# Optimization experiments

Measured on AMD Instinct MI355X. Metric: run time of the kernel, lower is better.

The kernel has to match this reference:

```python
import jax, jax.numpy as jnp
import numpy as np

B, C, H, W = 8, 256, 48, 48
RED = 1  # reduction
CR = C // RED
CG = C // 4  # fuse gate hidden channels


def conv1x1(x, w):
    # x: [B,C,H,W], w: [O,C] -> [B,O,H,W]
    return jnp.einsum('oc,bchw->bohw', w, x)


def conv3x3(x, w, b):
    # x: [B,Ci,H,W], w: [O,Ci,3,3], b: [O]
    y = jax.lax.conv_general_dilated(
        x, w, window_strides=(1, 1), padding='SAME',
        dimension_numbers=('NCHW', 'OIHW', 'NCHW'))
    return y + b[None, :, None, None]


def cross_attention(source, guidance, wq, wk, wv, bv, gamma):
    b, c, h, w = source.shape
    hw = h * w
    Q = conv1x1(source, wq).reshape(b, -1, hw)      # [B,CR,HW]
    K = conv1x1(guidance, wk).reshape(b, -1, hw)    # [B,CR,HW]
    V = (conv1x1(guidance, wv) + bv[None, :, None, None]).reshape(b, c, hw)
    energy = jnp.einsum('bqn,bqm->bnm', Q, K)       # [B,HW,HW]
    attn = jax.nn.softmax(energy, axis=-1)
    out = jnp.einsum('bcm,bnm->bcn', V, attn)       # [B,C,HW]
    return gamma * out.reshape(b, c, h, w) + source


def setup_inputs() -> dict:
    key = jax.random.key(0)
    ks = jax.random.split(key, 16)
    s = lambda fan_in: 1.0 / np.sqrt(fan_in)
    d = {
        'x1': jax.random.normal(ks[0], (B, C, H, W), jnp.float32),
        'x2': jax.random.normal(ks[1], (B, C, H, W), jnp.float32),
        'wq1': jax.random.normal(ks[2], (CR, C), jnp.float32) * s(C),
        'wk1': jax.random.normal(ks[3], (CR, C), jnp.float32) * s(C),
        'wv1': jax.random.normal(ks[4], (C, C), jnp.float32) * s(C),
        'bv1': jax.random.normal(ks[5], (C,), jnp.float32) * s(C),
        'gamma1': jax.random.normal(ks[6], (1,), jnp.float32) * 0.1,
        'wq2': jax.random.normal(ks[7], (CR, C), jnp.float32) * s(C),
        'wk2': jax.random.normal(ks[8], (CR, C), jnp.float32) * s(C),
        'wv2': jax.random.normal(ks[9], (C, C), jnp.float32) * s(C),
        'bv2': jax.random.normal(ks[10], (C,), jnp.float32) * s(C),
        'gamma2': jax.random.normal(ks[11], (1,), jnp.float32) * 0.1,
        'fw1': jax.random.normal(ks[12], (CG, 2 * C, 3, 3), jnp.float32) * s(2 * C * 9),
        'fb1': jnp.zeros((CG,), jnp.float32),
        'fw2': jax.random.normal(ks[13], (2, CG, 3, 3), jnp.float32) * s(CG * 9),
        'fb2': jnp.zeros((2,), jnp.float32),
    }
    return d


def reference(x1, x2, wq1, wk1, wv1, bv1, gamma1, wq2, wk2, wv2, bv2, gamma2,
              fw1, fb1, fw2, fb2):
    att_x1 = cross_attention(x1, x2, wq1, wk1, wv1, bv1, gamma1)
    att_x2 = cross_attention(x2, x1, wq2, wk2, wv2, bv2, gamma2)
    cat = jnp.concatenate([att_x1, att_x2], axis=1)  # [B,2C,H,W]
    h = jax.nn.relu(conv3x3(cat, fw1, fb1))
    gates = jax.nn.softmax(conv3x3(h, fw2, fb2), axis=1)  # [B,2,H,W]
    return gates[:, 0:1] * att_x1 + gates[:, 1:2] * att_x2
```

## Files before the change

kernel.cpp:

```cpp
#include <hip/hip_runtime.h>

namespace {

constexpr int BATCH = 8;
constexpr int CH    = 256;
constexpr int HW    = 2304;
constexpr int IMG   = 48;
constexpr int CG    = 64;

typedef __bf16 bf16x8 __attribute__((ext_vector_type(8)));
typedef __bf16 bf16x4 __attribute__((ext_vector_type(4)));
typedef float  f32x4  __attribute__((ext_vector_type(4)));

constexpr int ROWB = 40;
constexpr int PSTRD = 136;
constexpr int CSTR = 40;
constexpr int KQ_ELE = 8192;

constexpr size_t BF_SLAB = (size_t)BATCH * HW * CH * 2;
constexpr size_t QT1_OFF = 0;
constexpr size_t KT1_OFF = 1 * BF_SLAB;
constexpr size_t VB1_OFF = 2 * BF_SLAB;
constexpr size_t QT2_OFF = 3 * BF_SLAB;
constexpr size_t KT2_OFF = 4 * BF_SLAB;
constexpr size_t VB2_OFF = 5 * BF_SLAB;
constexpr size_t AT_OFF  = 6 * BF_SLAB;
constexpr size_t A1_OFF  = AT_OFF + (size_t)BATCH * HW * 512 * 2;
constexpr size_t A2_OFF  = A1_OFF + (size_t)BATCH * CH * HW * 4;
constexpr size_t HB_OFF  = A2_OFF + (size_t)BATCH * CH * HW * 4;
constexpr size_t G0_OFF  = HB_OFF + (size_t)BATCH * CG * HW * 4;
constexpr size_t WT_OFF  = G0_OFF + (size_t)BATCH * HW * 4;

__device__ __forceinline__ void dma16(const __bf16* g, __bf16* l) {
    __builtin_amdgcn_global_load_lds(
        (const __attribute__((address_space(1))) void*)g,
        (__attribute__((address_space(3))) void*)l,
        16, 0, 0);
}

__device__ __forceinline__ void issue_k_dma(const __bf16* __restrict__ KTb,
                                            __bf16* Kslot, int m0_i, int qq,
                                            int w, int lane) {
    const int lrow = lane >> 3;
    const int lg   = (lane & 7) ^ lrow;
    const int colb = qq * 64 + lg * 8;
#pragma unroll
    for (int qi = 0; qi < 4; ++qi) {
        const int row = (w * 4 + qi) * 8 + lrow;
        dma16(KTb + (size_t)(m0_i + row) * CH + colb,
              Kslot + (w * 4 + qi) * 512);
    }
}

__device__ __forceinline__ void stage_f32(const float* __restrict__ src, size_t srcStride,
                                          __bf16* dst, int t) {
    const int r = t & 127, s = t >> 7;
    const float4* sp = reinterpret_cast<const float4*>(src + (size_t)r * srcStride + s * 16);
    float4 f0 = sp[0], f1 = sp[1], f2 = sp[2], f3 = sp[3];
    bf16x8 v0, v1;
    v0[0]=(__bf16)f0.x; v0[1]=(__bf16)f0.y; v0[2]=(__bf16)f0.z; v0[3]=(__bf16)f0.w;
    v0[4]=(__bf16)f1.x; v0[5]=(__bf16)f1.y; v0[6]=(__bf16)f1.z; v0[7]=(__bf16)f1.w;
    v1[0]=(__bf16)f2.x; v1[1]=(__bf16)f2.y; v1[2]=(__bf16)f2.z; v1[3]=(__bf16)f2.w;
    v1[4]=(__bf16)f3.x; v1[5]=(__bf16)f3.y; v1[6]=(__bf16)f3.z; v1[7]=(__bf16)f3.w;
    bf16x8* dp = reinterpret_cast<bf16x8*>(dst + r * ROWB + s * 16);
    dp[0] = v0;
    dp[1] = v1;
}

__device__ __forceinline__ void frag_step(const __bf16* As, const __bf16* Bs,
                                          f32x4 (&acc)[4][4], int lane, int wm, int wn) {
    const int r = lane & 15, g = lane >> 4;
    bf16x8 a[4], b[4];
#pragma unroll
    for (int i = 0; i < 4; ++i) {
        a[i] = *reinterpret_cast<const bf16x8*>(As + (wm * 64 + i * 16 + r) * ROWB + g * 8);
        b[i] = *reinterpret_cast<const bf16x8*>(Bs + (wn * 64 + i * 16 + r) * ROWB + g * 8);
    }
#pragma unroll
    for (int i = 0; i < 4; ++i)
#pragma unroll
        for (int j = 0; j < 4; ++j)
            acc[i][j] = __builtin_amdgcn_mfma_f32_16x16x32_bf16(a[i], b[j], acc[i][j], 0, 0, 0);
}

__global__ __launch_bounds__(256) void proj3_mfma(
    const float* __restrict__ Xsrc, const float* __restrict__ Xg,
    const float* __restrict__ wq, const float* __restrict__ wk,
    const float* __restrict__ wv, const float* __restrict__ bv,
    __bf16* __restrict__ QT, __bf16* __restrict__ KT, __bf16* __restrict__ VB)
{
    __shared__ __bf16 As[128 * ROWB];
    __shared__ __bf16 Bs[128 * ROWB];
    const int p = blockIdx.z >> 3;
    const int b = blockIdx.z & 7;
    const float* W = (p == 0) ? wq : (p == 1) ? wk : wv;
    const float* X = (p == 0) ? Xsrc : Xg;
    const float* Xb = X + (size_t)b * CH * HW;

    const int t = threadIdx.x;
    const int lane = t & 63, wid = t >> 6;
    const int wm = wid >> 1, wn = wid & 1;
    const int m0 = blockIdx.y * 128, n0 = blockIdx.x * 128;

    f32x4 acc[4][4] = {};
    const int nB = t & 127, halfB = t >> 7;

    for (int k0 = 0; k0 < CH; k0 += 32) {
        stage_f32(W + (size_t)m0 * CH + k0, CH, As, t);
        float v[16];
#pragma unroll
        for (int kk = 0; kk < 16; ++kk)
            v[kk] = Xb[(size_t)(k0 + halfB * 16 + kk) * HW + n0 + nB];
        bf16x8 p0, p1;
#pragma unroll
        for (int kk = 0; kk < 8; ++kk) { p0[kk] = (__bf16)v[kk]; p1[kk] = (__bf16)v[kk + 8]; }
        bf16x8* dp = reinterpret_cast<bf16x8*>(Bs + nB * ROWB + halfB * 16);
        dp[0] = p0; dp[1] = p1;
        __syncthreads();
        frag_step(As, Bs, acc, lane, wm, wn);
        __syncthreads();
    }

    const int g = lane >> 4, r = lane & 15;
    if (p < 2) {
        __bf16* T = (p == 0) ? QT : KT;
#pragma unroll
        for (int mi = 0; mi < 4; ++mi)
#pragma unroll
            for (int nj = 0; nj < 4; ++nj) {
                const int mb = m0 + wm * 64 + mi * 16 + g * 4;
                const int n  = n0 + wn * 64 + nj * 16 + r;
                bf16x4 pk;
#pragma unroll
                for (int q = 0; q < 4; ++q) pk[q] = (__bf16)acc[mi][nj][q];
                *reinterpret_cast<bf16x4*>(T + ((size_t)b * HW + n) * CH + mb) = pk;
            }
    } else {
#pragma unroll
        for (int mi = 0; mi < 4; ++mi)
#pragma unroll
            for (int nj = 0; nj < 4; ++nj) {
                const int mb = m0 + wm * 64 + mi * 16 + g * 4;
                const int n  = n0 + wn * 64 + nj * 16 + r;
#pragma unroll
                for (int q = 0; q < 4; ++q)
                    VB[((size_t)b * CH + mb + q) * HW + n] = (__bf16)(acc[mi][nj][q] + bv[mb + q]);
            }
    }
}

__global__ __launch_bounds__(256, 2) void fused_flash(
    const __bf16* __restrict__ QT1, const __bf16* __restrict__ KT1, const __bf16* __restrict__ VB1,
    const __bf16* __restrict__ QT2, const __bf16* __restrict__ KT2, const __bf16* __restrict__ VB2,
    const float* __restrict__ x1, const float* __restrict__ x2,
    const float* __restrict__ g1, const float* __restrict__ g2,
    float* __restrict__ A1, float* __restrict__ A2, __bf16* __restrict__ AT)
{
    __shared__ __bf16 Ks[3 * KQ_ELE];
    __shared__ __bf16 P_lds[64 * PSTRD];
    __shared__ float  sc_lds[64];

    const int bid  = blockIdx.x;
    const int work = (bid & 7) * 72 + (bid >> 3);
    const int z = work / 36, ntile = work - z * 36;

    const int att = z >> 3, b = z & 7;
    const __bf16* QT = att ? QT2 : QT1;
    const __bf16* KT = att ? KT2 : KT1;
    const __bf16* VB = att ? VB2 : VB1;
    const float* src = att ? x2 : x1;
    const float* gmp = att ? g2 : g1;
    float* A         = att ? A2 : A1;
    const int aoff   = att ? CH : 0;

    const int t = threadIdx.x, lane = t & 63, w = t >> 6;
    const int r = lane & 15, g = lane >> 4;
    const int rs7 = r & 7;
    const int n0 = ntile * 64;
    const __bf16* KTb = KT + (size_t)b * HW * CH;
    const __bf16* VBb = VB + (size_t)b * CH * HW;

    bf16x8 qf[8];
    {
        const __bf16* qrow = QT + ((size_t)b * HW + n0 + w * 16 + r) * CH;
#pragma unroll
        for (int kc = 0; kc < 8; ++kc)
            qf[kc] = *reinterpret_cast<const bf16x8*>(qrow + kc * 32 + g * 8);
    }

    issue_k_dma(KTb, Ks, 0, 0, w, lane);
    issue_k_dma(KTb, Ks + KQ_ELE, 0, 1, w, lane);

    float m_run = -3.0e38f;
    float s_run = 0.f;
    f32x4 accO[4][4] = {};
    int base_t = 0;

    for (int tile = 0; tile < 18; ++tile) {
        const int m0 = tile * 128;
        f32x4 accS[8] = {};
#pragma unroll
        for (int q = 0; q < 4; ++q) {
            asm volatile("s_waitcnt vmcnt(4)\n\ts_barrier" ::: "memory");
            {
                int qq_i = q + 2;
                int m0_i = m0;
                if (qq_i >= 4) { qq_i -= 4; m0_i = (tile == 17) ? 0 : m0 + 128; }
                int slot_i = base_t + q + 2;
                if (slot_i >= 3) slot_i -= 3;
                if (slot_i >= 3) slot_i -= 3;
                issue_k_dma(KTb, Ks + slot_i * KQ_ELE, m0_i, qq_i, w, lane);
            }
            int slot = base_t + q;
            if (slot >= 3) slot -= 3;
            const __bf16* Kq = Ks + slot * KQ_ELE;
            __builtin_amdgcn_s_setprio(1);
#pragma unroll
            for (int kk = 0; kk < 2; ++kk) {
                const bf16x8 qv = qf[q * 2 + kk];
                const int swz = ((kk * 4 + g) ^ rs7) * 8;
#pragma unroll
                for (int j = 0; j < 8; ++j) {
                    const bf16x8 kf = *reinterpret_cast<const bf16x8*>(
                        Kq + (j * 16 + r) * 64 + swz);
                    accS[j] = __builtin_amdgcn_mfma_f32_16x16x32_bf16(kf, qv, accS[j], 0, 0, 0);
                }
            }
            __builtin_amdgcn_s_setprio(0);
        }
        {
            float mj[8];
#pragma unroll
            for (int j = 0; j < 8; ++j)
                mj[j] = fmaxf(fmaxf(accS[j][0], accS[j][1]), fmaxf(accS[j][2], accS[j][3]));
            float m03 = fmaxf(fmaxf(mj[0], mj[1]), fmaxf(mj[2], mj[3]));
            float m47 = fmaxf(fmaxf(mj[4], mj[5]), fmaxf(mj[6], mj[7]));
            float tmax = fmaxf(m03, m47);
            tmax = fmaxf(tmax, __shfl_xor(tmax, 16));
            tmax = fmaxf(tmax, __shfl_xor(tmax, 32));
            const float nm = fmaxf(m_run, tmax);
            float tsj[8];
#pragma unroll
            for (int j = 0; j < 8; ++j) {
                const float pe0 = __expf(accS[j][0] - nm);
                const float pe1 = __expf(accS[j][1] - nm);
                const float pe2 = __expf(accS[j][2] - nm);
                const float pe3 = __expf(accS[j][3] - nm);
                tsj[j] = (pe0 + pe1) + (pe2 + pe3);
                bf16x4 pk;
                pk[0] = (__bf16)pe0; pk[1] = (__bf16)pe1;
                pk[2] = (__bf16)pe2; pk[3] = (__bf16)pe3;
                *reinterpret_cast<bf16x4*>(
                    P_lds + (w * 16 + r) * PSTRD + j * 16 + g * 4) = pk;
            }
            float ts = ((tsj[0] + tsj[1]) + (tsj[2] + tsj[3])) +
                       ((tsj[4] + tsj[5]) + (tsj[6] + tsj[7]));
            ts += __shfl_xor(ts, 16);
            ts += __shfl_xor(ts, 32);
            const float scale = __expf(m_run - nm);
            s_run = s_run * scale + ts;
            m_run = nm;
            if (lane < 16) sc_lds[w * 16 + r] = scale;
        }
        asm volatile("s_waitcnt lgkmcnt(0)\n\ts_barrier" ::: "memory");
        {
            float scj[4];
#pragma unroll
            for (int j = 0; j < 4; ++j) scj[j] = sc_lds[j * 16 + r];
#pragma unroll
            for (int i = 0; i < 4; ++i)
#pragma unroll
                for (int j = 0; j < 4; ++j)
#pragma unroll
                    for (int q = 0; q < 4; ++q) accO[i][j][q] *= scj[j];
        }
        __builtin_amdgcn_s_setprio(1);
#pragma unroll
        for (int half = 0; half < 2; ++half) {
#pragma unroll
            for (int kk = 0; kk < 2; ++kk) {
                bf16x8 av[4], bp[4];
#pragma unroll
                for (int i = 0; i < 4; ++i)
                    av[i] = *reinterpret_cast<const bf16x8*>(
                        VBb + (size_t)(w * 64 + i * 16 + r) * HW + m0 + half * 64 + kk * 32 + g * 8);
#pragma unroll
                for (int j = 0; j < 4; ++j)
                    bp[j] = *reinterpret_cast<const bf16x8*>(
                        P_lds + (j * 16 + r) * PSTRD + half * 64 + kk * 32 + g * 8);
#pragma unroll
                for (int i = 0; i < 4; ++i)
#pragma unroll
                    for (int j = 0; j < 4; ++j)
                        accO[i][j] = __builtin_amdgcn_mfma_f32_16x16x32_bf16(
                            av[i], bp[j], accO[i][j], 0, 0, 0);
            }
        }
        __builtin_amdgcn_s_setprio(0);
        base_t += 1;
        if (base_t == 3) base_t = 0;
    }

    if (lane < 16) sc_lds[w * 16 + r] = 1.f / s_run;
    __syncthreads();
    float IS_l[4];
#pragma unroll
    for (int j = 0; j < 4; ++j) IS_l[j] = sc_lds[j * 16 + r];
    const float gm = gmp[0];
#pragma unroll
    for (int i = 0; i < 4; ++i)
#pragma unroll
        for (int j = 0; j < 4; ++j) {
            const int cb = w * 64 + i * 16 + g * 4;
            const int n  = n0 + j * 16 + r;
            const float sc = gm * IS_l[j];
            float vals[4];
#pragma unroll
            for (int q = 0; q < 4; ++q) {
                const size_t idx = ((size_t)b * CH + cb + q) * HW + n;
                vals[q] = sc * accO[i][j][q] + src[idx];
                A[idx] = vals[q];
            }
            bf16x4 pk;
#pragma unroll
            for (int q = 0; q < 4; ++q) pk[q] = (__bf16)vals[q];
            *reinterpret_cast<bf16x4*>(AT + ((size_t)b * HW + n) * 512 + aoff + cb) = pk;
        }
}

__global__ __launch_bounds__(256) void wprep(const float* __restrict__ fw1,
                                             __bf16* __restrict__ WT)
{
    const int i = blockIdx.x * 256 + threadIdx.x;
    const int tap = i >> 15;
    const int rem = i & 32767;
    const int m = rem >> 9, c = rem & 511;
    WT[i] = (__bf16)fw1[(size_t)m * 4608 + c * 9 + tap];
}

__global__ __launch_bounds__(256) void conv1_v2(
    const __bf16* __restrict__ AT, const __bf16* __restrict__ WT,
    float* __restrict__ P4)
{
    __shared__ __bf16 A9[9 * 64 * CSTR];
    __shared__ __bf16 HALO[240 * CSTR];
    const int kc = blockIdx.y, b = blockIdx.z, n0 = blockIdx.x * 128;
    const int t = threadIdx.x, lane = t & 63, wid = t >> 6;
    const int r = lane & 15, g = lane >> 4;

    int yj[2], xj[2];
#pragma unroll
    for (int j = 0; j < 2; ++j) {
        const int p = n0 + wid * 32 + j * 16 + r;
        yj[j] = p / IMG; xj[j] = p - yj[j] * IMG;
    }

    f32x4 acc[4][2] = {};

#pragma unroll 1
    for (int st = 0; st < 4; ++st) {
        const int cbase = kc * 128 + st * 32;
        if (t < 240) {
            const int nn = n0 - 56 + t;
            bf16x8 h0 = {}, h1 = {}, h2 = {}, h3 = {};
            if (nn >= 0 && nn < HW) {
                const bf16x8* sp = reinterpret_cast<const bf16x8*>(
                    AT + ((size_t)b * HW + nn) * 512 + cbase);
                h0 = sp[0]; h1 = sp[1]; h2 = sp[2]; h3 = sp[3];
            }
            bf16x8* dp = reinterpret_cast<bf16x8*>(HALO + t * CSTR);
            dp[0] = h0; dp[1] = h1; dp[2] = h2; dp[3] = h3;
        }
        {
            const int m = t >> 2, seg = t & 3;
#pragma unroll
            for (int tap = 0; tap < 9; ++tap)
                *reinterpret_cast<bf16x8*>(A9 + (tap * 64 + m) * CSTR + seg * 8) =
                    *reinterpret_cast<const bf16x8*>(WT + ((size_t)tap * 64 + m) * 512 + cbase + seg * 8);
        }
        __syncthreads();
#pragma unroll 1
        for (int tap = 0; tap < 9; ++tap) {
            const int dy = tap / 3 - 1;
            const int dx = tap - (tap / 3) * 3 - 1;
            bf16x8 bb[2];
#pragma unroll
            for (int j = 0; j < 2; ++j) {
                const bool valid = ((unsigned)(yj[j] + dy) < (unsigned)IMG) &&
                                   ((unsigned)(xj[j] + dx) < (unsigned)IMG);
                const int row = wid * 32 + j * 16 + r + 56 + dy * IMG + dx;
                bf16x8 v = {};
                if (valid) v = *reinterpret_cast<const bf16x8*>(HALO + row * CSTR + g * 8);
                bb[j] = v;
            }
            bf16x8 a[4];
#pragma unroll
            for (int i = 0; i < 4; ++i)
                a[i] = *reinterpret_cast<const bf16x8*>(A9 + (tap * 64 + i * 16 + r) * CSTR + g * 8);
#pragma unroll
            for (int i = 0; i < 4; ++i)
#pragma unroll
                for (int j = 0; j < 2; ++j)
                    acc[i][j] = __builtin_amdgcn_mfma_f32_16x16x32_bf16(a[i], bb[j], acc[i][j], 0, 0, 0);
        }
        __syncthreads();
    }
#pragma unroll
    for (int mi = 0; mi < 4; ++mi)
#pragma unroll
        for (int nj = 0; nj < 2; ++nj) {
            const int m = mi * 16 + g * 4;
            const int n = n0 + wid * 32 + nj * 16 + r;
#pragma unroll
            for (int q = 0; q < 4; ++q)
                P4[(((size_t)kc * BATCH + b) * CG + m + q) * HW + n] = acc[mi][nj][q];
        }
}

__global__ __launch_bounds__(256) void reduce_hb(
    const float* __restrict__ P4, const float* __restrict__ fb1,
    float* __restrict__ HB)
{
    const int idx = blockIdx.x * 256 + threadIdx.x;
    constexpr size_t STRIDE = (size_t)BATCH * CG * HW;
    const int m = (idx / HW) & 63;
    float s = P4[idx] + P4[idx + STRIDE] + P4[idx + 2 * STRIDE] + P4[idx + 3 * STRIDE];
    HB[idx] = fmaxf(s + fb1[m], 0.f);
}

__global__ __launch_bounds__(256) void gates_v2(
    const float* __restrict__ hbuf, const float* __restrict__ fw2,
    const float* __restrict__ fb2, float* __restrict__ g0buf)
{
    __shared__ float w2s[1152];
    __shared__ float par[2][4][64];
    const int t = threadIdx.x;
    for (int i = t; i < 1152; i += 256) w2s[i] = fw2[i];
    __syncthreads();
    const int px = t & 63, grp = t >> 6;
    const int idx = blockIdx.x * 64 + px;
    const int b = idx / HW;
    const int n = idx - b * HW;
    const int y = n / IMG, x = n - (n / IMG) * IMG;
    float c0 = 0.f, c1 = 0.f;
    const float* hb = hbuf + ((size_t)b * CG + grp * 16) * HW;
    for (int ci = 0; ci < 16; ++ci) {
        const float* hp = hb + (size_t)ci * HW;
        const float* w0 = &w2s[(grp * 16 + ci) * 9];
        const float* w1 = &w2s[576 + (grp * 16 + ci) * 9];
#pragma unroll
        for (int tap = 0; tap < 9; ++tap) {
            const int dy = tap / 3 - 1, dx = tap % 3 - 1;
            const int yy = y + dy, xx = x + dx;
            if (yy >= 0 && yy < IMG && xx >= 0 && xx < IMG) {
                const float hv = hp[yy * IMG + xx];
                c0 = fmaf(hv, w0[tap], c0);
                c1 = fmaf(hv, w1[tap], c1);
            }
        }
    }
    par[0][grp][px] = c0;
    par[1][grp][px] = c1;
    __syncthreads();
    if (t < 64) {
        const float s0 = par[0][0][t] + par[0][1][t] + par[0][2][t] + par[0][3][t] + fb2[0];
        const float s1 = par[1][0][t] + par[1][1][t] + par[1][2][t] + par[1][3][t] + fb2[1];
        g0buf[blockIdx.x * 64 + t] = 1.f / (1.f + __expf(s1 - s0));
    }
}

__global__ __launch_bounds__(256) void blend_kernel(
    const float* __restrict__ att1, const float* __restrict__ att2,
    const float* __restrict__ g0buf, float* __restrict__ out)
{
    const int i = blockIdx.x * 256 + threadIdx.x;
    const int r = i / 576;
    const int q = i - r * 576;
    const int b = r >> 8;
    const float4 a1 = reinterpret_cast<const float4*>(att1)[i];
    const float4 a2 = reinterpret_cast<const float4*>(att2)[i];
    const float4 g  = *reinterpret_cast<const float4*>(&g0buf[(size_t)b * HW + q * 4]);
    float4 o;
    o.x = g.x * a1.x + (1.f - g.x) * a2.x;
    o.y = g.y * a1.y + (1.f - g.y) * a2.y;
    o.z = g.z * a1.z + (1.f - g.z) * a2.z;
    o.w = g.w * a1.w + (1.f - g.w) * a2.w;
    reinterpret_cast<float4*>(out)[i] = o;
}

}

extern "C" void kernel_launch(void* const* d_in, const int* in_sizes, int n_in,
                              void* d_out, int out_size, void* d_ws, size_t ws_size,
                              hipStream_t stream)
{
    const float* x1  = (const float*)d_in[0];
    const float* x2  = (const float*)d_in[1];
    const float* wq1 = (const float*)d_in[2];
    const float* wk1 = (const float*)d_in[3];
    const float* wv1 = (const float*)d_in[4];
    const float* bv1 = (const float*)d_in[5];
    const float* g1  = (const float*)d_in[6];
    const float* wq2 = (const float*)d_in[7];
    const float* wk2 = (const float*)d_in[8];
    const float* wv2 = (const float*)d_in[9];
    const float* bv2 = (const float*)d_in[10];
    const float* g2  = (const float*)d_in[11];
    const float* fw1 = (const float*)d_in[12];
    const float* fb1 = (const float*)d_in[13];
    const float* fw2 = (const float*)d_in[14];
    const float* fb2 = (const float*)d_in[15];
    float* out = (float*)d_out;
    char*  wsb = (char*)d_ws;

    __bf16* QT1 = (__bf16*)(wsb + QT1_OFF);
    __bf16* KT1 = (__bf16*)(wsb + KT1_OFF);
    __bf16* VB1 = (__bf16*)(wsb + VB1_OFF);
    __bf16* QT2 = (__bf16*)(wsb + QT2_OFF);
    __bf16* KT2 = (__bf16*)(wsb + KT2_OFF);
    __bf16* VB2 = (__bf16*)(wsb + VB2_OFF);
    __bf16* AT  = (__bf16*)(wsb + AT_OFF);
    float*  A1  = (float*)(wsb + A1_OFF);
    float*  A2  = (float*)(wsb + A2_OFF);
    float*  HB  = (float*)(wsb + HB_OFF);
    float*  G0  = (float*)(wsb + G0_OFF);
    __bf16* WT  = (__bf16*)(wsb + WT_OFF);
    float*  P4  = (float*)(wsb + QT1_OFF);

    (void)in_sizes; (void)n_in; (void)out_size; (void)ws_size;

    proj3_mfma<<<dim3(18, 2, 24), 256, 0, stream>>>(x1, x2, wq1, wk1, wv1, bv1, QT1, KT1, VB1);
    proj3_mfma<<<dim3(18, 2, 24), 256, 0, stream>>>(x2, x1, wq2, wk2, wv2, bv2, QT2, KT2, VB2);
    wprep<<<dim3(1152), 256, 0, stream>>>(fw1, WT);

    fused_flash<<<dim3(576), 256, 0, stream>>>(
        QT1, KT1, VB1, QT2, KT2, VB2, x1, x2, g1, g2, A1, A2, AT);

    conv1_v2<<<dim3(18, 4, 8), 256, 0, stream>>>(AT, WT, P4);
    reduce_hb<<<dim3(4608), 256, 0, stream>>>(P4, fb1, HB);
    gates_v2<<<dim3(288), 256, 0, stream>>>(HB, fw2, fb2, G0);
    blend_kernel<<<dim3(4608), 256, 0, stream>>>(A1, A2, G0, out);
}
```

Before: 404.1 us.

## Keep attention probabilities in registers and read K directly from global memory

Removes all shared memory from the fused flash-attention kernel. K tiles are now loaded straight from global memory instead of through a triple-buffered DMA ring, and the probability tile is permuted between lanes with shuffles instead of being staged in LDS. Each wave now owns its 16 queries across all 256 channels, which removes the block barriers. The cost is that every wave reloads the full K and V tiles from global memory (four times the traffic), and the epilogue writes are scalar and less coalesced.

```diff
diff --git a/kernel.cpp b/kernel.cpp
--- a/kernel.cpp
+++ b/kernel.cpp
@@ -11,11 +11,10 @@
 typedef __bf16 bf16x8 __attribute__((ext_vector_type(8)));
 typedef __bf16 bf16x4 __attribute__((ext_vector_type(4)));
 typedef float  f32x4  __attribute__((ext_vector_type(4)));
+typedef unsigned u32x4 __attribute__((ext_vector_type(4)));
 
 constexpr int ROWB = 40;
-constexpr int PSTRD = 136;
 constexpr int CSTR = 40;
-constexpr int KQ_ELE = 8192;
 
 constexpr size_t BF_SLAB = (size_t)BATCH * HW * CH * 2;
 constexpr size_t QT1_OFF = 0;
@@ -31,25 +30,10 @@
 constexpr size_t G0_OFF  = HB_OFF + (size_t)BATCH * CG * HW * 4;
 constexpr size_t WT_OFF  = G0_OFF + (size_t)BATCH * HW * 4;
 
-__device__ __forceinline__ void dma16(const __bf16* g, __bf16* l) {
-    __builtin_amdgcn_global_load_lds(
-        (const __attribute__((address_space(1))) void*)g,
-        (__attribute__((address_space(3))) void*)l,
-        16, 0, 0);
-}
-
-__device__ __forceinline__ void issue_k_dma(const __bf16* __restrict__ KTb,
-                                            __bf16* Kslot, int m0_i, int qq,
-                                            int w, int lane) {
-    const int lrow = lane >> 3;
-    const int lg   = (lane & 7) ^ lrow;
-    const int colb = qq * 64 + lg * 8;
-#pragma unroll
-    for (int qi = 0; qi < 4; ++qi) {
-        const int row = (w * 4 + qi) * 8 + lrow;
-        dma16(KTb + (size_t)(m0_i + row) * CH + colb,
-              Kslot + (w * 4 + qi) * 512);
-    }
+__device__ __forceinline__ unsigned pk2(float lo, float hi) {
+    unsigned short a = __builtin_bit_cast(unsigned short, (__bf16)lo);
+    unsigned short b = __builtin_bit_cast(unsigned short, (__bf16)hi);
+    return (unsigned)a | ((unsigned)b << 16);
 }
 
 __device__ __forceinline__ void stage_f32(const float* __restrict__ src, size_t srcStride,
@@ -156,10 +140,6 @@
     const float* __restrict__ g1, const float* __restrict__ g2,
     float* __restrict__ A1, float* __restrict__ A2, __bf16* __restrict__ AT)
 {
-    __shared__ __bf16 Ks[3 * KQ_ELE];
-    __shared__ __bf16 P_lds[64 * PSTRD];
-    __shared__ float  sc_lds[64];
-
     const int bid  = blockIdx.x;
     const int work = (bid & 7) * 72 + (bid >> 3);
     const int z = work / 36, ntile = work - z * 36;
@@ -175,11 +155,13 @@
 
     const int t = threadIdx.x, lane = t & 63, w = t >> 6;
     const int r = lane & 15, g = lane >> 4;
-    const int rs7 = r & 7;
     const int n0 = ntile * 64;
     const __bf16* KTb = KT + (size_t)b * HW * CH;
     const __bf16* VBb = VB + (size_t)b * CH * HW;
 
+    const int sb  = r + (((lane >> 4) & 1) << 5);
+    const bool ghi = ((lane >> 5) & 1);
+
     bf16x8 qf[8];
     {
         const __bf16* qrow = QT + ((size_t)b * HW + n0 + w * 16 + r) * CH;
@@ -188,46 +170,25 @@
             qf[kc] = *reinterpret_cast<const bf16x8*>(qrow + kc * 32 + g * 8);
     }
 
-    issue_k_dma(KTb, Ks, 0, 0, w, lane);
-    issue_k_dma(KTb, Ks + KQ_ELE, 0, 1, w, lane);
-
     float m_run = -3.0e38f;
     float s_run = 0.f;
-    f32x4 accO[4][4] = {};
-    int base_t = 0;
+    f32x4 accO2[16] = {};
 
     for (int tile = 0; tile < 18; ++tile) {
         const int m0 = tile * 128;
         f32x4 accS[8] = {};
 #pragma unroll
-        for (int q = 0; q < 4; ++q) {
-            asm volatile("s_waitcnt vmcnt(4)\n\ts_barrier" ::: "memory");
-            {
-                int qq_i = q + 2;
-                int m0_i = m0;
-                if (qq_i >= 4) { qq_i -= 4; m0_i = (tile == 17) ? 0 : m0 + 128; }
-                int slot_i = base_t + q + 2;
-                if (slot_i >= 3) slot_i -= 3;
-                if (slot_i >= 3) slot_i -= 3;
-                issue_k_dma(KTb, Ks + slot_i * KQ_ELE, m0_i, qq_i, w, lane);
-            }
-            int slot = base_t + q;
-            if (slot >= 3) slot -= 3;
-            const __bf16* Kq = Ks + slot * KQ_ELE;
-            __builtin_amdgcn_s_setprio(1);
-#pragma unroll
-            for (int kk = 0; kk < 2; ++kk) {
-                const bf16x8 qv = qf[q * 2 + kk];
-                const int swz = ((kk * 4 + g) ^ rs7) * 8;
-#pragma unroll
-                for (int j = 0; j < 8; ++j) {
-                    const bf16x8 kf = *reinterpret_cast<const bf16x8*>(
-                        Kq + (j * 16 + r) * 64 + swz);
-                    accS[j] = __builtin_amdgcn_mfma_f32_16x16x32_bf16(kf, qv, accS[j], 0, 0, 0);
-                }
-            }
-            __builtin_amdgcn_s_setprio(0);
-        }
+        for (int kk = 0; kk < 8; ++kk) {
+            const bf16x8 qv = qf[kk];
+#pragma unroll
+            for (int j = 0; j < 8; ++j) {
+                const bf16x8 kf = *reinterpret_cast<const bf16x8*>(
+                    KTb + (size_t)(m0 + j * 16 + r) * CH + kk * 32 + g * 8);
+                accS[j] = __builtin_amdgcn_mfma_f32_16x16x32_bf16(kf, qv, accS[j], 0, 0, 0);
+            }
+        }
+        unsigned dwj[8][2];
+        float scale;
         {
             float mj[8];
 #pragma unroll
@@ -247,85 +208,74 @@
                 const float pe2 = __expf(accS[j][2] - nm);
                 const float pe3 = __expf(accS[j][3] - nm);
                 tsj[j] = (pe0 + pe1) + (pe2 + pe3);
-                bf16x4 pk;
-                pk[0] = (__bf16)pe0; pk[1] = (__bf16)pe1;
-                pk[2] = (__bf16)pe2; pk[3] = (__bf16)pe3;
-                *reinterpret_cast<bf16x4*>(
-                    P_lds + (w * 16 + r) * PSTRD + j * 16 + g * 4) = pk;
+                dwj[j][0] = pk2(pe0, pe1);
+                dwj[j][1] = pk2(pe2, pe3);
             }
             float ts = ((tsj[0] + tsj[1]) + (tsj[2] + tsj[3])) +
                        ((tsj[4] + tsj[5]) + (tsj[6] + tsj[7]));
             ts += __shfl_xor(ts, 16);
             ts += __shfl_xor(ts, 32);
-            const float scale = __expf(m_run - nm);
+            scale = __expf(m_run - nm);
             s_run = s_run * scale + ts;
             m_run = nm;
-            if (lane < 16) sc_lds[w * 16 + r] = scale;
-        }
-        asm volatile("s_waitcnt lgkmcnt(0)\n\ts_barrier" ::: "memory");
+        }
         {
-            float scj[4];
-#pragma unroll
-            for (int j = 0; j < 4; ++j) scj[j] = sc_lds[j * 16 + r];
-#pragma unroll
-            for (int i = 0; i < 4; ++i)
-#pragma unroll
-                for (int j = 0; j < 4; ++j)
-#pragma unroll
-                    for (int q = 0; q < 4; ++q) accO[i][j][q] *= scj[j];
+            float sc4[4];
+#pragma unroll
+            for (int q = 0; q < 4; ++q) sc4[q] = __shfl(scale, g * 4 + q);
+#pragma unroll
+            for (int cb = 0; cb < 16; ++cb)
+#pragma unroll
+                for (int q = 0; q < 4; ++q) accO2[cb][q] *= sc4[q];
+        }
+        bf16x8 pa[4];
+#pragma unroll
+        for (int ks = 0; ks < 4; ++ks) {
+            const unsigned a0 = (unsigned)__shfl((int)dwj[2 * ks][0], sb);
+            const unsigned b0 = (unsigned)__shfl((int)dwj[2 * ks + 1][0], sb);
+            const unsigned a1 = (unsigned)__shfl((int)dwj[2 * ks][1], sb);
+            const unsigned b1 = (unsigned)__shfl((int)dwj[2 * ks + 1][1], sb);
+            const unsigned a2 = (unsigned)__shfl((int)dwj[2 * ks][0], sb + 16);
+            const unsigned b2 = (unsigned)__shfl((int)dwj[2 * ks + 1][0], sb + 16);
+            const unsigned a3 = (unsigned)__shfl((int)dwj[2 * ks][1], sb + 16);
+            const unsigned b3 = (unsigned)__shfl((int)dwj[2 * ks + 1][1], sb + 16);
+            u32x4 dd;
+            dd.x = ghi ? b0 : a0;
+            dd.y = ghi ? b1 : a1;
+            dd.z = ghi ? b2 : a2;
+            dd.w = ghi ? b3 : a3;
+            pa[ks] = __builtin_bit_cast(bf16x8, dd);
         }
         __builtin_amdgcn_s_setprio(1);
 #pragma unroll
-        for (int half = 0; half < 2; ++half) {
-#pragma unroll
-            for (int kk = 0; kk < 2; ++kk) {
-                bf16x8 av[4], bp[4];
-#pragma unroll
-                for (int i = 0; i < 4; ++i)
-                    av[i] = *reinterpret_cast<const bf16x8*>(
-                        VBb + (size_t)(w * 64 + i * 16 + r) * HW + m0 + half * 64 + kk * 32 + g * 8);
-#pragma unroll
-                for (int j = 0; j < 4; ++j)
-                    bp[j] = *reinterpret_cast<const bf16x8*>(
-                        P_lds + (j * 16 + r) * PSTRD + half * 64 + kk * 32 + g * 8);
-#pragma unroll
-                for (int i = 0; i < 4; ++i)
-#pragma unroll
-                    for (int j = 0; j < 4; ++j)
-                        accO[i][j] = __builtin_amdgcn_mfma_f32_16x16x32_bf16(
-                            av[i], bp[j], accO[i][j], 0, 0, 0);
+        for (int cb = 0; cb < 16; ++cb) {
+#pragma unroll
+            for (int ks = 0; ks < 4; ++ks) {
+                const bf16x8 vf = *reinterpret_cast<const bf16x8*>(
+                    VBb + (size_t)(cb * 16 + r) * HW + m0 + ks * 32 + g * 8);
+                accO2[cb] = __builtin_amdgcn_mfma_f32_16x16x32_bf16(pa[ks], vf, accO2[cb], 0, 0, 0);
             }
         }
         __builtin_amdgcn_s_setprio(0);
-        base_t += 1;
-        if (base_t == 3) base_t = 0;
-    }
-
-    if (lane < 16) sc_lds[w * 16 + r] = 1.f / s_run;
-    __syncthreads();
-    float IS_l[4];
-#pragma unroll
-    for (int j = 0; j < 4; ++j) IS_l[j] = sc_lds[j * 16 + r];
+    }
+
+    const float inv = 1.f / s_run;
+    float is4[4];
+#pragma unroll
+    for (int q = 0; q < 4; ++q) is4[q] = __shfl(inv, g * 4 + q);
     const float gm = gmp[0];
 #pragma unroll
-    for (int i = 0; i < 4; ++i)
-#pragma unroll
-        for (int j = 0; j < 4; ++j) {
-            const int cb = w * 64 + i * 16 + g * 4;
-            const int n  = n0 + j * 16 + r;
-            const float sc = gm * IS_l[j];
-            float vals[4];
-#pragma unroll
-            for (int q = 0; q < 4; ++q) {
-                const size_t idx = ((size_t)b * CH + cb + q) * HW + n;
-                vals[q] = sc * accO[i][j][q] + src[idx];
-                A[idx] = vals[q];
-            }
-            bf16x4 pk;
-#pragma unroll
-            for (int q = 0; q < 4; ++q) pk[q] = (__bf16)vals[q];
-            *reinterpret_cast<bf16x4*>(AT + ((size_t)b * HW + n) * 512 + aoff + cb) = pk;
-        }
+    for (int cb = 0; cb < 16; ++cb) {
+        const int c = cb * 16 + r;
+#pragma unroll
+        for (int q = 0; q < 4; ++q) {
+            const int n = n0 + w * 16 + g * 4 + q;
+            const size_t idx = ((size_t)b * CH + c) * HW + n;
+            const float val = gm * is4[q] * accO2[cb][q] + src[idx];
+            A[idx] = val;
+            AT[((size_t)b * HW + n) * 512 + aoff + c] = (__bf16)val;
+        }
+    }
 }
 
 __global__ __launch_bounds__(256) void wprep(const float* __restrict__ fw1,
```

Result: slower. 1.032 ms (+155.5%).
